# Kernel tuning notes

Measured on AMD Instinct MI355X. Metric: run time of the kernel, lower is better.

Reference implementation:

```python
import jax, jax.numpy as jnp
import numpy as np

B = 20000      # batch (edges/nodes)
DIM = 512      # irreps feature dim for x, y, and out
NNZ = 5000     # number of nonzero CG paths


def setup_inputs() -> dict:
    key = jax.random.key(0)
    k1, k2, k3, k4, k5, k6 = jax.random.split(key, 6)
    x = jax.random.normal(k1, (B, DIM), dtype=jnp.float32)
    y = jax.random.normal(k2, (B, DIM), dtype=jnp.float32)
    scale = jax.random.normal(k3, (NNZ,), dtype=jnp.float32)  # CG coefficients
    M = jnp.sort(jax.random.randint(k4, (NNZ,), 0, DIM, dtype=jnp.int32))   # scatter idx into out
    M1 = jax.random.randint(k5, (NNZ,), 0, DIM, dtype=jnp.int32)            # gather idx into x
    M2 = jax.random.randint(k6, (NNZ,), 0, DIM, dtype=jnp.int32)            # gather idx into y
    return {"x": x, "y": y, "scale": scale, "M": M, "M1": M1, "M2": M2}


def reference(x, y, scale, M, M1, M2):
    # sparse_mul: out[b, M[i]] += scale[i] * x[b, M1[i]] * y[b, M2[i]]
    prod = x[:, M1] * y[:, M2] * scale[None, :]          # [B, NNZ]
    out = jnp.zeros((x.shape[0], DIM), dtype=x.dtype)
    out = out.at[:, M].add(prod)                          # scatter-accumulate over feature axis
    return out
```

## Files before the change

### kernel.cpp

```cpp
#include <hip/hip_runtime.h>
#include <hip/hip_fp16.h>


#define BLK    256
#define RROWS  8
#define DIMC   512
#define DEPTH  8
#define SLOTS  256


__global__ void prep_kernel(const float* __restrict__ scale,
                            const int* __restrict__ M,
                            const int* __restrict__ M1,
                            const int* __restrict__ M2,
                            int2* __restrict__ pk2, int* __restrict__ starts,
                            int nnz)
{
    int i = blockIdx.x * blockDim.x + threadIdx.x;
    if (i < nnz) {
        unsigned key = (unsigned)M[i] | ((unsigned)M1[i] << 10)
                                      | ((unsigned)M2[i] << 20);
        pk2[i] = make_int2((int)key, __float_as_int(scale[i]));
    }
    if (i <= SLOTS) {
        int j = (int)((long long)i * nnz / SLOTS);
        if (j > 0 && j < nnz) {
            const int prev = M[j - 1];
            while (j < nnz && M[j] == prev) ++j;
        }
        if (j > nnz) j = nnz;
        starts[i] = j;
    }
}

__device__ __forceinline__ void fma8h(const uint4& xu, const uint4& yu,
                                      float s, float4& a0, float4& a1)
{
    const __half2 p0 = __hmul2(*(const __half2*)&xu.x, *(const __half2*)&yu.x);
    const __half2 p1 = __hmul2(*(const __half2*)&xu.y, *(const __half2*)&yu.y);
    const __half2 p2 = __hmul2(*(const __half2*)&xu.z, *(const __half2*)&yu.z);
    const __half2 p3 = __hmul2(*(const __half2*)&xu.w, *(const __half2*)&yu.w);
    a0.x = fmaf(s, __low2float(p0),  a0.x);
    a0.y = fmaf(s, __high2float(p0), a0.y);
    a0.z = fmaf(s, __low2float(p1),  a0.z);
    a0.w = fmaf(s, __high2float(p1), a0.w);
    a1.x = fmaf(s, __low2float(p2),  a1.x);
    a1.y = fmaf(s, __high2float(p2), a1.y);
    a1.z = fmaf(s, __low2float(p3),  a1.z);
    a1.w = fmaf(s, __high2float(p3), a1.w);
}

__global__ __launch_bounds__(BLK, 5) void sparse_mul_kernel(
    const float* __restrict__ x, const float* __restrict__ y,
    const int2* __restrict__ pk2, const int* __restrict__ starts,
    float* __restrict__ out, int B)
{
    __shared__ uint4  xs_u[DIMC];
    __shared__ uint4  ys_u[DIMC];
    __shared__ float4 os4[2 * DIMC];

    const int tid = threadIdx.x;
    const int b0  = blockIdx.x * RROWS;
    const bool full = (b0 + RROWS) <= B;

    #pragma unroll
    for (int f = tid; f < 2 * DIMC; f += BLK)
        os4[f] = make_float4(0.f, 0.f, 0.f, 0.f);

    for (int f = tid; f < DIMC; f += BLK) {
        const int d = f;
        float xr[RROWS], yr[RROWS];
        if (full) {
            #pragma unroll
            for (int r = 0; r < RROWS; ++r) {
                xr[r] = x[(size_t)(b0 + r) * DIMC + d];
                yr[r] = y[(size_t)(b0 + r) * DIMC + d];
            }
        } else {
            #pragma unroll
            for (int r = 0; r < RROWS; ++r) {
                const bool ok = (b0 + r) < B;
                xr[r] = ok ? x[(size_t)(b0 + r) * DIMC + d] : 0.f;
                yr[r] = ok ? y[(size_t)(b0 + r) * DIMC + d] : 0.f;
            }
        }
        uint4 xu, yu;
        {
            __half2 h0 = __floats2half2_rn(xr[0], xr[1]);
            __half2 h1 = __floats2half2_rn(xr[2], xr[3]);
            __half2 h2 = __floats2half2_rn(xr[4], xr[5]);
            __half2 h3 = __floats2half2_rn(xr[6], xr[7]);
            xu = make_uint4(*(unsigned*)&h0, *(unsigned*)&h1,
                            *(unsigned*)&h2, *(unsigned*)&h3);
            h0 = __floats2half2_rn(yr[0], yr[1]);
            h1 = __floats2half2_rn(yr[2], yr[3]);
            h2 = __floats2half2_rn(yr[4], yr[5]);
            h3 = __floats2half2_rn(yr[6], yr[7]);
            yu = make_uint4(*(unsigned*)&h0, *(unsigned*)&h1,
                            *(unsigned*)&h2, *(unsigned*)&h3);
        }
        xs_u[d] = xu;
        ys_u[d] = yu;
    }
    __syncthreads();

    const int i0 = starts[tid];
    const int ie = starts[tid + 1];

    if (i0 < ie) {
        const int last = ie - 1;

        int2 buf[DEPTH];
        #pragma unroll
        for (int j = 0; j < DEPTH; ++j) buf[j] = pk2[min(i0 + j, last)];

        float4 a0 = make_float4(0.f, 0.f, 0.f, 0.f);
        float4 a1 = make_float4(0.f, 0.f, 0.f, 0.f);

        int   mC = buf[0].x & 1023;
        int   sC = buf[0].y;
        uint4 xu = xs_u[((unsigned)buf[0].x >> 10) & 1023u];
        uint4 yu = ys_u[(unsigned)buf[0].x >> 20];
        int   cur = mC;

        for (int base = i0; base < ie; base += DEPTH) {
            int2 nxt[DEPTH];
            #pragma unroll
            for (int j = 0; j < DEPTH; ++j)
                nxt[j] = pk2[min(base + DEPTH + j, last)];

            #pragma unroll
            for (int j = 0; j < DEPTH; ++j) {
                const int2 ne = (j < DEPTH - 1) ? buf[j + 1] : nxt[0];
                const int   mN  = ne.x & 1023;
                const uint4 xuN = xs_u[((unsigned)ne.x >> 10) & 1023u];
                const uint4 yuN = ys_u[(unsigned)ne.x >> 20];

                if (mC != cur) {
                    os4[2 * cur]     = a0;
                    os4[2 * cur + 1] = a1;
                    a0 = make_float4(0.f, 0.f, 0.f, 0.f);
                    a1 = make_float4(0.f, 0.f, 0.f, 0.f);
                    cur = mC;
                }
                const float s = (base + j < ie) ? __int_as_float(sC) : 0.f;
                fma8h(xu, yu, s, a0, a1);

                mC = mN; sC = ne.y; xu = xuN; yu = yuN;
            }
            #pragma unroll
            for (int j = 0; j < DEPTH; ++j) buf[j] = nxt[j];
        }
        os4[2 * cur]     = a0;
        os4[2 * cur + 1] = a1;
    }
    __syncthreads();

    for (int f = tid; f < DIMC; f += BLK) {
        const int d = f;
        const float4 v0 = os4[2 * d];
        const float4 v1 = os4[2 * d + 1];
        if (full) {
            out[(size_t)(b0 + 0) * DIMC + d] = v0.x;
            out[(size_t)(b0 + 1) * DIMC + d] = v0.y;
            out[(size_t)(b0 + 2) * DIMC + d] = v0.z;
            out[(size_t)(b0 + 3) * DIMC + d] = v0.w;
            out[(size_t)(b0 + 4) * DIMC + d] = v1.x;
            out[(size_t)(b0 + 5) * DIMC + d] = v1.y;
            out[(size_t)(b0 + 6) * DIMC + d] = v1.z;
            out[(size_t)(b0 + 7) * DIMC + d] = v1.w;
        } else {
            const float vv[8] = {v0.x, v0.y, v0.z, v0.w, v1.x, v1.y, v1.z, v1.w};
            #pragma unroll
            for (int r = 0; r < RROWS; ++r)
                if ((b0 + r) < B) out[(size_t)(b0 + r) * DIMC + d] = vv[r];
        }
    }
}

__global__ void sparse_mul_fallback(
    const float* __restrict__ x, const float* __restrict__ y,
    const float* __restrict__ scale, const int* __restrict__ M,
    const int* __restrict__ M1, const int* __restrict__ M2,
    float* __restrict__ out, int nnz)
{
    __shared__ float orow[DIMC];
    const int b = blockIdx.x;
    for (int d = threadIdx.x; d < DIMC; d += blockDim.x) orow[d] = 0.f;
    __syncthreads();
    for (int i = threadIdx.x; i < nnz; i += blockDim.x) {
        const float v = scale[i] * x[(size_t)b * DIMC + M1[i]]
                                 * y[(size_t)b * DIMC + M2[i]];
        atomicAdd(&orow[M[i]], v);
    }
    __syncthreads();
    for (int d = threadIdx.x; d < DIMC; d += blockDim.x)
        out[(size_t)b * DIMC + d] = orow[d];
}

extern "C" void kernel_launch(void* const* d_in, const int* in_sizes, int n_in,
                              void* d_out, int out_size, void* d_ws, size_t ws_size,
                              hipStream_t stream) {
    const float* x     = (const float*)d_in[0];
    const float* y     = (const float*)d_in[1];
    const float* scale = (const float*)d_in[2];
    const int*   M     = (const int*)d_in[3];
    const int*   M1    = (const int*)d_in[4];
    const int*   M2    = (const int*)d_in[5];
    float* out = (float*)d_out;

    const int B   = in_sizes[0] / DIMC;
    const int nnz = in_sizes[2];

    const size_t need = (size_t)nnz * sizeof(int2) + (SLOTS + 1) * sizeof(int);
    if (nnz > 0 && ws_size >= need) {
        int2* pk2   = (int2*)d_ws;
        int* starts = (int*)((char*)d_ws + (size_t)nnz * sizeof(int2));
        const int pn = (nnz > SLOTS + 1) ? nnz : SLOTS + 1;
        prep_kernel<<<(pn + BLK - 1) / BLK, BLK, 0, stream>>>(
            scale, M, M1, M2, pk2, starts, nnz);
        const int grid = (B + RROWS - 1) / RROWS;
        sparse_mul_kernel<<<grid, BLK, 0, stream>>>(x, y, pk2, starts, out, B);
    } else {
        sparse_mul_fallback<<<B, BLK, 0, stream>>>(x, y, scale, M, M1, M2, out, nnz);
    }
}
```

Measured before the change: 151.6 us.

## Transpose padded CG path list into per-thread interleaved int4 layout with warp-uniform trip counts

Preprocessing now pads each thread's segment of CG paths to a per-wavefront maximum length and stores the entries transposed, so consecutive threads read consecutive int4 pairs. This makes the hot path-list loads coalesced, and the main loop runs a wave-uniform trip count without the per-element bounds select. Padding entries use a dummy key with zero scale and are not written back. In exchange it adds an extra prep kernel, a memset, and some wasted iterations on the padded entries, and it only applies when nnz is at most 6000. The old path is kept as a fallback, with its prefetch changed to a rolling one.

```diff
diff --git a/kernel.cpp b/kernel.cpp
--- a/kernel.cpp
+++ b/kernel.cpp
@@ -7,30 +7,59 @@
 #define DIMC   512
 #define DEPTH  8
 #define SLOTS  256
-
-
-__global__ void prep_kernel(const float* __restrict__ scale,
-                            const int* __restrict__ M,
-                            const int* __restrict__ M1,
-                            const int* __restrict__ M2,
-                            int2* __restrict__ pk2, int* __restrict__ starts,
-                            int nnz)
-{
-    int i = blockIdx.x * blockDim.x + threadIdx.x;
-    if (i < nnz) {
-        unsigned key = (unsigned)M[i] | ((unsigned)M1[i] << 10)
-                                      | ((unsigned)M2[i] << 20);
-        pk2[i] = make_int2((int)key, __float_as_int(scale[i]));
-    }
-    if (i <= SLOTS) {
-        int j = (int)((long long)i * nnz / SLOTS);
+#define KMAX   64
+#define KPAIRS 36
+#define PADKEY 1023
+
+
+
+__global__ void prep1_kernel(const int* __restrict__ M,
+                             int* __restrict__ hdr, int* __restrict__ starts,
+                             int nnz)
+{
+    const int i = blockIdx.x * blockDim.x + threadIdx.x;
+    if (i > SLOTS) return;
+    auto snap = [&](int v) -> int {
+        int j = (int)((long long)v * nnz / SLOTS);
         if (j > 0 && j < nnz) {
             const int prev = M[j - 1];
             while (j < nnz && M[j] == prev) ++j;
         }
         if (j > nnz) j = nnz;
-        starts[i] = j;
-    }
+        return j;
+    };
+    const int s0 = snap(i);
+    starts[i] = s0;
+    if (i < SLOTS) {
+        const int len = snap(i + 1) - s0;
+        atomicMax(&hdr[i >> 6], len);
+    }
+}
+
+__global__ void prep2_kernel(const float* __restrict__ scale,
+                             const int* __restrict__ M,
+                             const int* __restrict__ M1,
+                             const int* __restrict__ M2,
+                             const int* __restrict__ starts,
+                             int4* __restrict__ pk2Tp, int nnz)
+{
+    const int p   = blockIdx.x;
+    const int tid = threadIdx.x;
+    const int i0  = starts[tid];
+    const int len = starts[tid + 1] - i0;
+    const int k0  = 2 * p, k1 = 2 * p + 1;
+    int2 e0, e1;
+    if (k0 < len) {
+        const int idx = i0 + k0;
+        e0 = make_int2(M[idx] | (M1[idx] << 10) | (M2[idx] << 20),
+                       __float_as_int(scale[idx]));
+    } else e0 = make_int2(PADKEY, 0);
+    if (k1 < len) {
+        const int idx = i0 + k1;
+        e1 = make_int2(M[idx] | (M1[idx] << 10) | (M2[idx] << 20),
+                       __float_as_int(scale[idx]));
+    } else e1 = make_int2(PADKEY, 0);
+    pk2Tp[p * BLK + tid] = make_int4(e0.x, e0.y, e1.x, e1.y);
 }
 
 __device__ __forceinline__ void fma8h(const uint4& xu, const uint4& yu,
@@ -50,9 +79,10 @@
     a1.w = fmaf(s, __high2float(p3), a1.w);
 }
 
-__global__ __launch_bounds__(BLK, 5) void sparse_mul_kernel(
+
+__global__ __launch_bounds__(BLK, 5) void sparse_mul_t(
     const float* __restrict__ x, const float* __restrict__ y,
-    const int2* __restrict__ pk2, const int* __restrict__ starts,
+    const int* __restrict__ hdr, const int4* __restrict__ pk2Tp,
     float* __restrict__ out, int B)
 {
     __shared__ uint4  xs_u[DIMC];
@@ -63,7 +93,6 @@
     const int b0  = blockIdx.x * RROWS;
     const bool full = (b0 + RROWS) <= B;
 
-    #pragma unroll
     for (int f = tid; f < 2 * DIMC; f += BLK)
         os4[f] = make_float4(0.f, 0.f, 0.f, 0.f);
 
@@ -104,15 +133,17 @@
     }
     __syncthreads();
 
-    const int i0 = starts[tid];
-    const int ie = starts[tid + 1];
-
-    if (i0 < ie) {
-        const int last = ie - 1;
+    {
+        const int km = hdr[tid >> 6];
+        const int4* pp = pk2Tp + tid;
 
         int2 buf[DEPTH];
         #pragma unroll
-        for (int j = 0; j < DEPTH; ++j) buf[j] = pk2[min(i0 + j, last)];
+        for (int p = 0; p < DEPTH / 2; ++p) {
+            const int4 q = pp[p * BLK];
+            buf[2 * p]     = make_int2(q.x, q.y);
+            buf[2 * p + 1] = make_int2(q.z, q.w);
+        }
 
         float4 a0 = make_float4(0.f, 0.f, 0.f, 0.f);
         float4 a1 = make_float4(0.f, 0.f, 0.f, 0.f);
@@ -123,15 +154,10 @@
         uint4 yu = ys_u[(unsigned)buf[0].x >> 20];
         int   cur = mC;
 
-        for (int base = i0; base < ie; base += DEPTH) {
-            int2 nxt[DEPTH];
-            #pragma unroll
-            for (int j = 0; j < DEPTH; ++j)
-                nxt[j] = pk2[min(base + DEPTH + j, last)];
-
+        for (int k0 = 0; k0 < km; k0 += DEPTH) {
             #pragma unroll
             for (int j = 0; j < DEPTH; ++j) {
-                const int2 ne = (j < DEPTH - 1) ? buf[j + 1] : nxt[0];
+                const int2 ne = buf[(j + 1) & (DEPTH - 1)];
                 const int   mN  = ne.x & 1023;
                 const uint4 xuN = xs_u[((unsigned)ne.x >> 10) & 1023u];
                 const uint4 yuN = ys_u[(unsigned)ne.x >> 20];
@@ -143,16 +169,20 @@
                     a1 = make_float4(0.f, 0.f, 0.f, 0.f);
                     cur = mC;
                 }
-                const float s = (base + j < ie) ? __int_as_float(sC) : 0.f;
-                fma8h(xu, yu, s, a0, a1);
-
+                fma8h(xu, yu, __int_as_float(sC), a0, a1);
+
+                if ((j & 1) == 0) {
+                    const int4 q = pp[((k0 + DEPTH + j) >> 1) * BLK];
+                    buf[j]     = make_int2(q.x, q.y);
+                    buf[j + 1] = make_int2(q.z, q.w);
+                }
                 mC = mN; sC = ne.y; xu = xuN; yu = yuN;
             }
-            #pragma unroll
-            for (int j = 0; j < DEPTH; ++j) buf[j] = nxt[j];
-        }
-        os4[2 * cur]     = a0;
-        os4[2 * cur + 1] = a1;
+        }
+        if (cur != PADKEY) {
+            os4[2 * cur]     = a0;
+            os4[2 * cur + 1] = a1;
+        }
     }
     __syncthreads();
 
@@ -178,6 +208,124 @@
     }
 }
 
+
+__global__ void prep_r7(const float* __restrict__ scale,
+                        const int* __restrict__ M,
+                        const int* __restrict__ M1,
+                        const int* __restrict__ M2,
+                        int2* __restrict__ pk2, int* __restrict__ starts,
+                        int nnz)
+{
+    int i = blockIdx.x * blockDim.x + threadIdx.x;
+    if (i < nnz) {
+        unsigned key = (unsigned)M[i] | ((unsigned)M1[i] << 10)
+                                      | ((unsigned)M2[i] << 20);
+        pk2[i] = make_int2((int)key, __float_as_int(scale[i]));
+    }
+    if (i <= SLOTS) {
+        int j = (int)((long long)i * nnz / SLOTS);
+        if (j > 0 && j < nnz) {
+            const int prev = M[j - 1];
+            while (j < nnz && M[j] == prev) ++j;
+        }
+        if (j > nnz) j = nnz;
+        starts[i] = j;
+    }
+}
+
+__global__ __launch_bounds__(BLK, 5) void sparse_mul_r7(
+    const float* __restrict__ x, const float* __restrict__ y,
+    const int2* __restrict__ pk2, const int* __restrict__ starts,
+    float* __restrict__ out, int B)
+{
+    __shared__ uint4  xs_u[DIMC];
+    __shared__ uint4  ys_u[DIMC];
+    __shared__ float4 os4[2 * DIMC];
+
+    const int tid = threadIdx.x;
+    const int b0  = blockIdx.x * RROWS;
+    const bool full = (b0 + RROWS) <= B;
+
+    for (int f = tid; f < 2 * DIMC; f += BLK)
+        os4[f] = make_float4(0.f, 0.f, 0.f, 0.f);
+
+    for (int f = tid; f < DIMC; f += BLK) {
+        const int d = f;
+        float xr[RROWS], yr[RROWS];
+        #pragma unroll
+        for (int r = 0; r < RROWS; ++r) {
+            const bool ok = full || (b0 + r) < B;
+            xr[r] = ok ? x[(size_t)(b0 + r) * DIMC + d] : 0.f;
+            yr[r] = ok ? y[(size_t)(b0 + r) * DIMC + d] : 0.f;
+        }
+        __half2 h0 = __floats2half2_rn(xr[0], xr[1]);
+        __half2 h1 = __floats2half2_rn(xr[2], xr[3]);
+        __half2 h2 = __floats2half2_rn(xr[4], xr[5]);
+        __half2 h3 = __floats2half2_rn(xr[6], xr[7]);
+        xs_u[d] = make_uint4(*(unsigned*)&h0, *(unsigned*)&h1,
+                             *(unsigned*)&h2, *(unsigned*)&h3);
+        h0 = __floats2half2_rn(yr[0], yr[1]);
+        h1 = __floats2half2_rn(yr[2], yr[3]);
+        h2 = __floats2half2_rn(yr[4], yr[5]);
+        h3 = __floats2half2_rn(yr[6], yr[7]);
+        ys_u[d] = make_uint4(*(unsigned*)&h0, *(unsigned*)&h1,
+                             *(unsigned*)&h2, *(unsigned*)&h3);
+    }
+    __syncthreads();
+
+    const int i0 = starts[tid];
+    const int ie = starts[tid + 1];
+
+    if (i0 < ie) {
+        const int last = ie - 1;
+        int2 buf[DEPTH];
+        #pragma unroll
+        for (int j = 0; j < DEPTH; ++j) buf[j] = pk2[min(i0 + j, last)];
+
+        float4 a0 = make_float4(0.f, 0.f, 0.f, 0.f);
+        float4 a1 = make_float4(0.f, 0.f, 0.f, 0.f);
+        int   mC = buf[0].x & 1023;
+        int   sC = buf[0].y;
+        uint4 xu = xs_u[((unsigned)buf[0].x >> 10) & 1023u];
+        uint4 yu = ys_u[(unsigned)buf[0].x >> 20];
+        int   cur = mC;
+
+        for (int base = i0; base < ie; base += DEPTH) {
+            #pragma unroll
+            for (int j = 0; j < DEPTH; ++j) {
+                const int2 ne = buf[(j + 1) & (DEPTH - 1)];
+                const int   mN  = ne.x & 1023;
+                const uint4 xuN = xs_u[((unsigned)ne.x >> 10) & 1023u];
+                const uint4 yuN = ys_u[(unsigned)ne.x >> 20];
+                if (mC != cur) {
+                    os4[2 * cur]     = a0;
+                    os4[2 * cur + 1] = a1;
+                    a0 = make_float4(0.f, 0.f, 0.f, 0.f);
+                    a1 = make_float4(0.f, 0.f, 0.f, 0.f);
+                    cur = mC;
+                }
+                const float s = (base + j < ie) ? __int_as_float(sC) : 0.f;
+                fma8h(xu, yu, s, a0, a1);
+                buf[j] = pk2[min(base + DEPTH + j, last)];
+                mC = mN; sC = ne.y; xu = xuN; yu = yuN;
+            }
+        }
+        os4[2 * cur]     = a0;
+        os4[2 * cur + 1] = a1;
+    }
+    __syncthreads();
+
+    for (int f = tid; f < DIMC; f += BLK) {
+        const int d = f;
+        const float4 v0 = os4[2 * d];
+        const float4 v1 = os4[2 * d + 1];
+        const float vv[8] = {v0.x, v0.y, v0.z, v0.w, v1.x, v1.y, v1.z, v1.w};
+        #pragma unroll
+        for (int r = 0; r < RROWS; ++r)
+            if (full || (b0 + r) < B) out[(size_t)(b0 + r) * DIMC + d] = vv[r];
+    }
+}
+
 __global__ void sparse_mul_fallback(
     const float* __restrict__ x, const float* __restrict__ y,
     const float* __restrict__ scale, const int* __restrict__ M,
@@ -212,15 +360,27 @@
     const int B   = in_sizes[0] / DIMC;
     const int nnz = in_sizes[2];
 
-    const size_t need = (size_t)nnz * sizeof(int2) + (SLOTS + 1) * sizeof(int);
-    if (nnz > 0 && ws_size >= need) {
+    const int grid = (B + RROWS - 1) / RROWS;
+
+    const size_t needT  = 1056 + (size_t)KPAIRS * BLK * sizeof(int4);
+    const size_t needR7 = (size_t)nnz * sizeof(int2) + (SLOTS + 1) * sizeof(int);
+
+    if (nnz > 0 && nnz <= 6000 && ws_size >= needT) {
+        int*  hdr    = (int*)d_ws;
+        int*  starts = (int*)((char*)d_ws + 16);
+        int4* pk2Tp  = (int4*)((char*)d_ws + 1056);
+        hipMemsetAsync(hdr, 0, 16, stream);
+        prep1_kernel<<<2, BLK, 0, stream>>>(M, hdr, starts, nnz);
+        prep2_kernel<<<KPAIRS, BLK, 0, stream>>>(scale, M, M1, M2, starts,
+                                                 pk2Tp, nnz);
+        sparse_mul_t<<<grid, BLK, 0, stream>>>(x, y, hdr, pk2Tp, out, B);
+    } else if (nnz > 0 && ws_size >= needR7) {
         int2* pk2   = (int2*)d_ws;
         int* starts = (int*)((char*)d_ws + (size_t)nnz * sizeof(int2));
         const int pn = (nnz > SLOTS + 1) ? nnz : SLOTS + 1;
-        prep_kernel<<<(pn + BLK - 1) / BLK, BLK, 0, stream>>>(
+        prep_r7<<<(pn + BLK - 1) / BLK, BLK, 0, stream>>>(
             scale, M, M1, M2, pk2, starts, nnz);
-        const int grid = (B + RROWS - 1) / RROWS;
-        sparse_mul_kernel<<<grid, BLK, 0, stream>>>(x, y, pk2, starts, out, B);
+        sparse_mul_r7<<<grid, BLK, 0, stream>>>(x, y, pk2, starts, out, B);
     } else {
         sparse_mul_fallback<<<B, BLK, 0, stream>>>(x, y, scale, M, M1, M2, out, nnz);
     }
```

New measurement: 152.5 us. No clear change (+0.6%).
